# Performance work log

Measured on AMD Instinct MI355X. Metric: run time of the kernel, lower is better.

Reference implementation:

```python
import jax, jax.numpy as jnp
import numpy as np

D_EMB = 1024
N_HEAD = 16
D_K = D_EMB // N_HEAD


def setup_inputs() -> dict:
    key = jax.random.key(0)
    ks = jax.random.split(key, 11)
    B, S = 2, 2048
    s = 1.0 / np.sqrt(D_EMB)
    inp = {
        'Q': jax.random.normal(ks[0], (B, S, D_EMB), jnp.float32),
        'K': jax.random.normal(ks[1], (B, S, D_EMB), jnp.float32),
        'V': jax.random.normal(ks[2], (B, S, D_EMB), jnp.float32),
        'W_Q': jax.random.normal(ks[3], (D_EMB, D_EMB), jnp.float32) * s,
        'b_Q': jax.random.normal(ks[4], (D_EMB,), jnp.float32) * s,
        'W_K': jax.random.normal(ks[5], (D_EMB, D_EMB), jnp.float32) * s,
        'b_K': jax.random.normal(ks[6], (D_EMB,), jnp.float32) * s,
        'W_V': jax.random.normal(ks[7], (D_EMB, D_EMB), jnp.float32) * s,
        'b_V': jax.random.normal(ks[8], (D_EMB,), jnp.float32) * s,
        'W_O': jax.random.normal(ks[9], (D_EMB, D_EMB), jnp.float32) * s,
        'b_O': jax.random.normal(ks[10], (D_EMB,), jnp.float32) * s,
    }
    return inp


def _heads(x):
    # [B, S, D] -> [B, H, S, d_k]
    B, S, _ = x.shape
    return x.reshape(B, S, N_HEAD, D_K).transpose(0, 2, 1, 3)


def reference(Q, K, V, W_Q, b_Q, W_K, b_K, W_V, b_V, W_O, b_O):
    q = _heads(Q @ W_Q.T + b_Q)
    k = _heads(K @ W_K.T + b_K)
    v = _heads(V @ W_V.T + b_V)
    scale = 1.0 / jnp.sqrt(jnp.asarray(D_K, q.dtype))
    scores = jnp.einsum('bhqd,bhkd->bhqk', q, k) * scale  # [B,H,S,S]
    probs = jax.nn.softmax(scores, axis=-1)
    attn = jnp.einsum('bhqk,bhkd->bhqd', probs, v)
    B, H, S, d = attn.shape
    attn = attn.transpose(0, 2, 1, 3).reshape(B, S, H * d)
    return attn @ W_O.T + b_O
```

## Files before the change

kernel.cpp:

```cpp
#include <hip/hip_runtime.h>
#include <cstdint>
#include <cstddef>

#define S_LEN 2048
#define NH    16
#define DKH   64
#define DEMB  1024
#define MTOT  4096

typedef float f32x4 __attribute__((ext_vector_type(4)));
typedef __bf16 bf16x8 __attribute__((ext_vector_type(8)));
typedef _Float16 f16;
typedef f16 f16x2 __attribute__((ext_vector_type(2)));
typedef f16 f16x4 __attribute__((ext_vector_type(4)));
typedef unsigned short u16;
typedef unsigned int u32;
typedef u16 u16x8 __attribute__((ext_vector_type(8)));
typedef u16 u16x4 __attribute__((ext_vector_type(4)));

static __device__ __forceinline__ u16 f2bf(float f) {
  u32 u = __builtin_bit_cast(u32, f);
  u += 0x7fffu + ((u >> 16) & 1u);
  return (u16)(u >> 16);
}
static __device__ __forceinline__ float bf2f(u16 b) {
  return __builtin_bit_cast(float, ((u32)b) << 16);
}
static __device__ __forceinline__ bf16x8 ldfrag(const u16* p) {
  return __builtin_bit_cast(bf16x8, *(const u16x8*)p);
}
static __device__ __forceinline__ f16x4 ldfragh(const u16* p) {
  return __builtin_bit_cast(f16x4, *(const u16x4*)p);
}
static __device__ __forceinline__ f32x4 mfma16(bf16x8 a, bf16x8 b, f32x4 c) {
  return __builtin_amdgcn_mfma_f32_16x16x32_bf16(a, b, c, 0, 0, 0);
}
static __device__ __forceinline__ f32x4 mfmah(f16x4 a, f16x4 b, f32x4 c) {
  return __builtin_amdgcn_mfma_f32_16x16x16f16(a, b, c, 0, 0, 0);
}
static __device__ __forceinline__ void gl2lds16(const void* g, void* l) {
  __builtin_amdgcn_global_load_lds((__attribute__((address_space(1))) void*)g,
                                   (__attribute__((address_space(3))) void*)l,
                                   16, 0, 0);
}
static __device__ __forceinline__ f16x4 pkh4(float a, float b, float c, float d) {
  f16x2 lo = __builtin_bit_cast(f16x2, __builtin_amdgcn_cvt_pkrtz(a, b));
  f16x2 hi = __builtin_bit_cast(f16x2, __builtin_amdgcn_cvt_pkrtz(c, d));
  return __builtin_shufflevector(lo, hi, 0, 1, 2, 3);
}

#define SCL_Q (0.125f * 1.44269504088896340736f)

__global__ __launch_bounds__(256) void cvt_all(
    const float* __restrict__ wq, const float* __restrict__ wk,
    const float* __restrict__ wv, const float* __restrict__ wo,
    const float* __restrict__ q, const float* __restrict__ k,
    const float* __restrict__ v, u16* __restrict__ dW, u16* __restrict__ dA) {
  int b = blockIdx.x;
  const float* s; u16* d;
  if (b < 4096) {
    const int seg = b >> 10;
    s = (seg == 0) ? wq : (seg == 1) ? wk : (seg == 2) ? wv : wo;
    d = dW + (size_t)seg * (DEMB * DEMB);
    b &= 1023;
  } else {
    const int bb = b - 4096;
    const int seg = bb >> 12;
    s = (seg == 0) ? q : (seg == 1) ? k : v;
    d = dA + (size_t)seg * ((size_t)MTOT * DEMB);
    b = bb & 4095;
  }
  const int i = (b * 256 + threadIdx.x) * 4;
  f32x4 f = *(const f32x4*)(s + i);
  u16x4 o;
  o[0] = f2bf(f[0]); o[1] = f2bf(f[1]); o[2] = f2bf(f[2]); o[3] = f2bf(f[3]);
  *(u16x4*)(d + i) = o;
}

__global__ __launch_bounds__(256) void qkv_gemm(
    const u16* __restrict__ qin, const u16* __restrict__ kin,
    const u16* __restrict__ vin, const u16* __restrict__ W,
    const float* __restrict__ bq, const float* __restrict__ bk,
    const float* __restrict__ bv,
    u16* __restrict__ qh, u16* __restrict__ kh, u16* __restrict__ vt) {
  __shared__ __align__(16) u16 sA[128 * 32];
  __shared__ __align__(16) u16 sB[128 * 32];
  const int t = threadIdx.x;
  const int l = t & 63, w = t >> 6;
  const int ll = l & 15, lg = l >> 4;
  const int nb = blockIdx.x;
  const int mb = blockIdx.y;
  const int which = nb >> 3;
  const u16* A = (which == 0) ? qin : ((which == 1) ? kin : vin);
  const int wr = (w >> 1) * 64, wc = (w & 1) * 64;

  f32x4 acc[4][4] = {};

  for (int kt = 0; kt < 32; ++kt) {
    const int k0 = kt * 32;
    __syncthreads();
#pragma unroll
    for (int i = 0; i < 2; ++i) {
      const int c = i * 256 + t;
      const int row = c >> 2;
      const int gc = (c & 3) ^ ((row >> 1) & 3);
      gl2lds16(A + (size_t)(mb * 128 + row) * DEMB + k0 + gc * 8, &sA[c * 8]);
      gl2lds16(W + (size_t)(nb * 128 + row) * DEMB + k0 + gc * 8, &sB[c * 8]);
    }
    __syncthreads();

    bf16x8 af[4], bfr[4];
#pragma unroll
    for (int i2 = 0; i2 < 4; ++i2) {
      const int row = wr + i2 * 16 + ll;
      af[i2] = ldfrag(&sA[row * 32 + (lg ^ ((row >> 1) & 3)) * 8]);
    }
#pragma unroll
    for (int j2 = 0; j2 < 4; ++j2) {
      const int row = wc + j2 * 16 + ll;
      bfr[j2] = ldfrag(&sB[row * 32 + (lg ^ ((row >> 1) & 3)) * 8]);
    }
#pragma unroll
    for (int i2 = 0; i2 < 4; ++i2)
#pragma unroll
      for (int j2 = 0; j2 < 4; ++j2)
        acc[i2][j2] = mfma16(af[i2], bfr[j2], acc[i2][j2]);
  }

  const float* bias = (which == 0) ? bq : ((which == 1) ? bk : bv);
  const int b = (mb * 128) >> 11;

  if (which == 2) {
#pragma unroll
    for (int j2 = 0; j2 < 4; ++j2) {
      const int nl = (nb * 128 + wc + j2 * 16 + ll) & 1023;
      const int h = nl >> 6, dk = nl & 63;
      const float bb = bias[nl];
      u16* base = vt + ((size_t)((b * NH + h) * DKH + dk)) * S_LEN;
#pragma unroll
      for (int i2 = 0; i2 < 4; ++i2) {
        const int s = (mb * 128 + wr + i2 * 16 + lg * 4) & 2047;
        const f16x4 pk = pkh4(acc[i2][j2][0] + bb, acc[i2][j2][1] + bb,
                              acc[i2][j2][2] + bb, acc[i2][j2][3] + bb);
        *(u16x4*)&base[s] = __builtin_bit_cast(u16x4, pk);
      }
    }
  } else {
    u16* outp = (which == 0) ? qh : kh;
    const float scl = (which == 0) ? SCL_Q : 1.0f;
#pragma unroll
    for (int j2 = 0; j2 < 4; ++j2) {
      const int nl = (nb * 128 + wc + j2 * 16 + ll) & 1023;
      const int h = nl >> 6, dk = nl & 63;
      const float bb = bias[nl];
#pragma unroll
      for (int i2 = 0; i2 < 4; ++i2) {
#pragma unroll
        for (int r = 0; r < 4; ++r) {
          const int s = (mb * 128 + wr + i2 * 16 + lg * 4 + r) & 2047;
          const float val = (acc[i2][j2][r] + bb) * scl;
          outp[((size_t)((b * NH + h) * S_LEN + s)) * DKH + dk] = f2bf(val);
        }
      }
    }
  }
}

__global__ __launch_bounds__(256) void attn_kernel(
    const u16* __restrict__ qh, const u16* __restrict__ kh,
    const u16* __restrict__ vt, u16* __restrict__ opart,
    float* __restrict__ lpart) {
  __shared__ __align__(16) u16 sK[64 * 64];
  __shared__ __align__(16) u16 sV[64 * 64];
  const int t = threadIdx.x;
  const int l = t & 63, w = t >> 6;
  const int ll = l & 15, lg = l >> 4;
  const int qb = blockIdx.x >> 1;
  const int ks = blockIdx.x & 1;
  const int q_blk = qb * 128;
  const int bh = blockIdx.y;

  bf16x8 aq[2][2];
#pragma unroll
  for (int qt = 0; qt < 2; ++qt) {
    const u16* qbase = qh + ((size_t)bh * S_LEN + q_blk + w * 32 + qt * 16 + ll) * DKH;
    aq[qt][0] = ldfrag(qbase + lg * 8);
    aq[qt][1] = ldfrag(qbase + 32 + lg * 8);
  }

  f32x4 oT[2][4] = {};
  float l_part[2] = {0.f, 0.f};

  for (int kt = 0; kt < 16; ++kt) {
    const int kb0 = ks * 1024 + kt * 64;
    __syncthreads();
#pragma unroll
    for (int i = 0; i < 2; ++i) {
      const int c = i * 256 + t;
      const int row = c >> 3, gc = (c & 7) ^ (row & 7);
      gl2lds16(kh + ((size_t)bh * S_LEN + kb0 + row) * DKH + gc * 8,
               &sK[c * 8]);
      gl2lds16(vt + ((size_t)bh * DKH + row) * S_LEN + kb0 + gc * 8,
               &sV[c * 8]);
    }
    __syncthreads();

#pragma unroll
    for (int kbl = 0; kbl < 4; ++kbl) {
      const int krow = kbl * 16 + ll;
      const bf16x8 ak0 = ldfrag(&sK[krow * 64 + (lg ^ (ll & 7)) * 8]);
      const bf16x8 ak1 = ldfrag(&sK[krow * 64 + ((4 + lg) ^ (ll & 7)) * 8]);
      f32x4 s0 = {}, s1 = {};
      s0 = mfma16(ak0, aq[0][0], s0);
      s0 = mfma16(ak1, aq[0][1], s0);
      s1 = mfma16(ak0, aq[1][0], s1);
      s1 = mfma16(ak1, aq[1][1], s1);

      f16x4 bp0, bp1;
      {
        const float p0 = __builtin_amdgcn_exp2f(s0[0]);
        const float p1 = __builtin_amdgcn_exp2f(s0[1]);
        const float p2 = __builtin_amdgcn_exp2f(s0[2]);
        const float p3 = __builtin_amdgcn_exp2f(s0[3]);
        l_part[0] += (p0 + p1) + (p2 + p3);
        bp0 = pkh4(p0, p1, p2, p3);
      }
      {
        const float p0 = __builtin_amdgcn_exp2f(s1[0]);
        const float p1 = __builtin_amdgcn_exp2f(s1[1]);
        const float p2 = __builtin_amdgcn_exp2f(s1[2]);
        const float p3 = __builtin_amdgcn_exp2f(s1[3]);
        l_part[1] += (p0 + p1) + (p2 + p3);
        bp1 = pkh4(p0, p1, p2, p3);
      }

#pragma unroll
      for (int nt = 0; nt < 4; ++nt) {
        const int row = nt * 16 + ll;
        const int ch = (kbl * 2 + (lg >> 1)) ^ (ll & 7);
        const f16x4 av = ldfragh(&sV[row * 64 + ch * 8 + (lg & 1) * 4]);
        oT[0][nt] = mfmah(av, bp0, oT[0][nt]);
        oT[1][nt] = mfmah(av, bp1, oT[1][nt]);
      }
    }
  }

#pragma unroll
  for (int qt = 0; qt < 2; ++qt) {
    float lv = l_part[qt];
    lv += __shfl_xor(lv, 16, 64);
    lv += __shfl_xor(lv, 32, 64);
    const int srow = q_blk + w * 32 + qt * 16 + ll;
    u16* obase = opart + (((size_t)(ks * 32 + bh)) * S_LEN + srow) * DKH;
#pragma unroll
    for (int nt = 0; nt < 4; ++nt) {
      u16x4 o;
#pragma unroll
      for (int r = 0; r < 4; ++r) o[r] = f2bf(oT[qt][nt][r]);
      *(u16x4*)&obase[nt * 16 + lg * 4] = o;
    }
    if (lg == 0) lpart[(ks * 32 + bh) * S_LEN + srow] = lv;
  }
}

__global__ __launch_bounds__(256) void merge_ctx(
    const u16* __restrict__ op, const float* __restrict__ lp,
    u16* __restrict__ ctx) {
  const int idx = blockIdx.x * 256 + threadIdx.x;
  const int dk8 = idx & 7;
  const int q = (idx >> 3) & 2047;
  const int bh = idx >> 14;
  const float inv = 1.0f / (lp[bh * S_LEN + q] + lp[(32 + bh) * S_LEN + q]);
  const u16x8 a = *(const u16x8*)&op[((size_t)bh * S_LEN + q) * DKH + dk8 * 8];
  const u16x8 c = *(const u16x8*)&op[((size_t)(32 + bh) * S_LEN + q) * DKH + dk8 * 8];
  u16x8 o;
#pragma unroll
  for (int r = 0; r < 8; ++r) o[r] = f2bf((bf2f(a[r]) + bf2f(c[r])) * inv);
  const int b = bh >> 4, h = bh & 15;
  *(u16x8*)&ctx[((size_t)((b * S_LEN + q) * NH + h)) * DKH + dk8 * 8] = o;
}

__global__ __launch_bounds__(256) void out_gemm(
    const u16* __restrict__ Am, const u16* __restrict__ W,
    const float* __restrict__ bo, float* __restrict__ out) {
  __shared__ __align__(16) u16 sA[64 * 64];
  __shared__ __align__(16) u16 sB[64 * 64];
  const int t = threadIdx.x;
  const int l = t & 63, w = t >> 6;
  const int ll = l & 15, lg = l >> 4;
  const int nb = blockIdx.x;
  const int mb = blockIdx.y;
  const int wr = (w >> 1) * 32, wc = (w & 1) * 32;

  f32x4 acc[2][2] = {};
  for (int kt = 0; kt < 16; ++kt) {
    const int k0 = kt * 64;
    __syncthreads();
#pragma unroll
    for (int i = 0; i < 2; ++i) {
      const int c = i * 256 + t;
      const int row = c >> 3;
      const int gc = (c & 7) ^ (row & 7);
      gl2lds16(Am + (size_t)(mb * 64 + row) * DEMB + k0 + gc * 8, &sA[c * 8]);
      gl2lds16(W + (size_t)(nb * 64 + row) * DEMB + k0 + gc * 8, &sB[c * 8]);
    }
    __syncthreads();
#pragma unroll
    for (int sub = 0; sub < 2; ++sub) {
      bf16x8 af[2], bfr[2];
#pragma unroll
      for (int i2 = 0; i2 < 2; ++i2) {
        const int row = wr + i2 * 16 + ll;
        af[i2] = ldfrag(&sA[row * 64 + ((sub * 4 + lg) ^ (row & 7)) * 8]);
      }
#pragma unroll
      for (int j2 = 0; j2 < 2; ++j2) {
        const int row = wc + j2 * 16 + ll;
        bfr[j2] = ldfrag(&sB[row * 64 + ((sub * 4 + lg) ^ (row & 7)) * 8]);
      }
#pragma unroll
      for (int i2 = 0; i2 < 2; ++i2)
#pragma unroll
        for (int j2 = 0; j2 < 2; ++j2)
          acc[i2][j2] = mfma16(af[i2], bfr[j2], acc[i2][j2]);
    }
  }

#pragma unroll
  for (int j2 = 0; j2 < 2; ++j2) {
    const int ncol = nb * 64 + wc + j2 * 16 + ll;
    const float bb = bo[ncol];
#pragma unroll
    for (int i2 = 0; i2 < 2; ++i2) {
#pragma unroll
      for (int r = 0; r < 4; ++r) {
        const int mrow = mb * 64 + wr + i2 * 16 + lg * 4 + r;
        out[(size_t)mrow * DEMB + ncol] = acc[i2][j2][r] + bb;
      }
    }
  }
}

extern "C" void kernel_launch(void* const* d_in, const int* in_sizes, int n_in,
                              void* d_out, int out_size, void* d_ws,
                              size_t ws_size, hipStream_t stream) {
  (void)in_sizes; (void)n_in; (void)out_size; (void)ws_size;
  const float* Q  = (const float*)d_in[0];
  const float* K  = (const float*)d_in[1];
  const float* V  = (const float*)d_in[2];
  const float* WQ = (const float*)d_in[3];
  const float* bQ = (const float*)d_in[4];
  const float* WK = (const float*)d_in[5];
  const float* bK = (const float*)d_in[6];
  const float* WV = (const float*)d_in[7];
  const float* bV = (const float*)d_in[8];
  const float* WO = (const float*)d_in[9];
  const float* bO = (const float*)d_in[10];
  float* out = (float*)d_out;

  u16* ws   = (u16*)d_ws;
  u16* Wqkv = ws;
  u16* Wo   = Wqkv + 3072 * 1024;
  u16* qin  = Wo + 1024 * 1024;
  u16* kin  = qin + (size_t)MTOT * DEMB;
  u16* vin  = kin + (size_t)MTOT * DEMB;
  u16* qh   = vin + (size_t)MTOT * DEMB;
  u16* kh   = qh + 32 * 2048 * 64;
  u16* vt   = kh + 32 * 2048 * 64;
  u16* ctx  = vt + 32 * 2048 * 64;
  u16* opart   = qin;
  float* lpart = (float*)Wqkv;

  cvt_all<<<16384, 256, 0, stream>>>(WQ, WK, WV, WO, Q, K, V, Wqkv, qin);

  qkv_gemm<<<dim3(24, 32), 256, 0, stream>>>(qin, kin, vin, Wqkv, bQ, bK, bV,
                                             qh, kh, vt);
  attn_kernel<<<dim3(32, 32), 256, 0, stream>>>(qh, kh, vt, opart, lpart);
  merge_ctx<<<2048, 256, 0, stream>>>(opart, lpart, ctx);
  out_gemm<<<dim3(16, 64), 256, 0, stream>>>(ctx, Wo, bO, out);
}
```

Baseline: 235.3 us.

## Double-buffer attention and output GEMM, enlarge K tiles and block sizes

The QKV GEMM moves from a 32-wide to a 64-wide K tile, halving the number of barrier-separated load/compute rounds. The attention kernel now uses 512-thread blocks covering 256 queries with double-buffered K/V tiles, so loads overlap MFMA work. The output GEMM grows to 128x64 tiles with double-buffered LDS. Together these aim to hide global-to-LDS latency and reduce synchronisation, at the cost of more LDS per block and possibly lower occupancy.

After: 233.4 us. No clear change (-0.8%).

```diff
diff --git a/kernel.cpp b/kernel.cpp
--- a/kernel.cpp
+++ b/kernel.cpp
@@ -83,8 +83,8 @@
     const float* __restrict__ bq, const float* __restrict__ bk,
     const float* __restrict__ bv,
     u16* __restrict__ qh, u16* __restrict__ kh, u16* __restrict__ vt) {
-  __shared__ __align__(16) u16 sA[128 * 32];
-  __shared__ __align__(16) u16 sB[128 * 32];
+  __shared__ __align__(16) u16 sA[128 * 64];
+  __shared__ __align__(16) u16 sB[128 * 64];
   const int t = threadIdx.x;
   const int l = t & 63, w = t >> 6;
   const int ll = l & 15, lg = l >> 4;
@@ -96,35 +96,38 @@
 
   f32x4 acc[4][4] = {};
 
-  for (int kt = 0; kt < 32; ++kt) {
-    const int k0 = kt * 32;
-    __syncthreads();
-#pragma unroll
-    for (int i = 0; i < 2; ++i) {
+  for (int kt = 0; kt < 16; ++kt) {
+    const int k0 = kt * 64;
+    __syncthreads();
+#pragma unroll
+    for (int i = 0; i < 4; ++i) {
       const int c = i * 256 + t;
-      const int row = c >> 2;
-      const int gc = (c & 3) ^ ((row >> 1) & 3);
+      const int row = c >> 3;
+      const int gc = (c & 7) ^ (row & 7);
       gl2lds16(A + (size_t)(mb * 128 + row) * DEMB + k0 + gc * 8, &sA[c * 8]);
       gl2lds16(W + (size_t)(nb * 128 + row) * DEMB + k0 + gc * 8, &sB[c * 8]);
     }
     __syncthreads();
 
-    bf16x8 af[4], bfr[4];
-#pragma unroll
-    for (int i2 = 0; i2 < 4; ++i2) {
-      const int row = wr + i2 * 16 + ll;
-      af[i2] = ldfrag(&sA[row * 32 + (lg ^ ((row >> 1) & 3)) * 8]);
-    }
-#pragma unroll
-    for (int j2 = 0; j2 < 4; ++j2) {
-      const int row = wc + j2 * 16 + ll;
-      bfr[j2] = ldfrag(&sB[row * 32 + (lg ^ ((row >> 1) & 3)) * 8]);
-    }
-#pragma unroll
-    for (int i2 = 0; i2 < 4; ++i2)
-#pragma unroll
-      for (int j2 = 0; j2 < 4; ++j2)
-        acc[i2][j2] = mfma16(af[i2], bfr[j2], acc[i2][j2]);
+#pragma unroll
+    for (int kk = 0; kk < 2; ++kk) {
+      bf16x8 af[4], bfr[4];
+#pragma unroll
+      for (int i2 = 0; i2 < 4; ++i2) {
+        const int row = wr + i2 * 16 + ll;
+        af[i2] = ldfrag(&sA[row * 64 + ((kk * 4 + lg) ^ (row & 7)) * 8]);
+      }
+#pragma unroll
+      for (int j2 = 0; j2 < 4; ++j2) {
+        const int row = wc + j2 * 16 + ll;
+        bfr[j2] = ldfrag(&sB[row * 64 + ((kk * 4 + lg) ^ (row & 7)) * 8]);
+      }
+#pragma unroll
+      for (int i2 = 0; i2 < 4; ++i2)
+#pragma unroll
+        for (int j2 = 0; j2 < 4; ++j2)
+          acc[i2][j2] = mfma16(af[i2], bfr[j2], acc[i2][j2]);
+    }
   }
 
   const float* bias = (which == 0) ? bq : ((which == 1) ? bk : bv);
@@ -166,24 +169,25 @@
   }
 }
 
-__global__ __launch_bounds__(256) void attn_kernel(
+__global__ __launch_bounds__(512, 4) void attn_kernel(
     const u16* __restrict__ qh, const u16* __restrict__ kh,
     const u16* __restrict__ vt, u16* __restrict__ opart,
     float* __restrict__ lpart) {
-  __shared__ __align__(16) u16 sK[64 * 64];
-  __shared__ __align__(16) u16 sV[64 * 64];
+  __shared__ __align__(16) u16 sK0[64 * 64], sK1[64 * 64];
+  __shared__ __align__(16) u16 sV0[64 * 64], sV1[64 * 64];
   const int t = threadIdx.x;
   const int l = t & 63, w = t >> 6;
   const int ll = l & 15, lg = l >> 4;
   const int qb = blockIdx.x >> 1;
   const int ks = blockIdx.x & 1;
-  const int q_blk = qb * 128;
+  const int q_blk = qb * 256;
   const int bh = blockIdx.y;
 
   bf16x8 aq[2][2];
 #pragma unroll
   for (int qt = 0; qt < 2; ++qt) {
-    const u16* qbase = qh + ((size_t)bh * S_LEN + q_blk + w * 32 + qt * 16 + ll) * DKH;
+    const u16* qbase =
+        qh + ((size_t)bh * S_LEN + q_blk + w * 32 + qt * 16 + ll) * DKH;
     aq[qt][0] = ldfrag(qbase + lg * 8);
     aq[qt][1] = ldfrag(qbase + 32 + lg * 8);
   }
@@ -191,25 +195,22 @@
   f32x4 oT[2][4] = {};
   float l_part[2] = {0.f, 0.f};
 
-  for (int kt = 0; kt < 16; ++kt) {
-    const int kb0 = ks * 1024 + kt * 64;
-    __syncthreads();
-#pragma unroll
-    for (int i = 0; i < 2; ++i) {
-      const int c = i * 256 + t;
-      const int row = c >> 3, gc = (c & 7) ^ (row & 7);
-      gl2lds16(kh + ((size_t)bh * S_LEN + kb0 + row) * DKH + gc * 8,
-               &sK[c * 8]);
-      gl2lds16(vt + ((size_t)bh * DKH + row) * S_LEN + kb0 + gc * 8,
-               &sV[c * 8]);
-    }
-    __syncthreads();
-
+  const int strow = t >> 3;
+  const int sgc = (t & 7) ^ (strow & 7);
+  const u16* kstg = kh + ((size_t)bh * S_LEN + ks * 1024 + strow) * DKH + sgc * 8;
+  const u16* vstg = vt + ((size_t)bh * DKH + strow) * S_LEN + ks * 1024 + sgc * 8;
+
+  auto stg = [&](int kt, u16* dK, u16* dV) {
+    gl2lds16(kstg + (size_t)kt * 64 * DKH, dK + t * 8);
+    gl2lds16(vstg + kt * 64, dV + t * 8);
+  };
+
+  auto compute = [&](const u16* cK, const u16* cV) {
 #pragma unroll
     for (int kbl = 0; kbl < 4; ++kbl) {
       const int krow = kbl * 16 + ll;
-      const bf16x8 ak0 = ldfrag(&sK[krow * 64 + (lg ^ (ll & 7)) * 8]);
-      const bf16x8 ak1 = ldfrag(&sK[krow * 64 + ((4 + lg) ^ (ll & 7)) * 8]);
+      const bf16x8 ak0 = ldfrag(&cK[krow * 64 + (lg ^ (ll & 7)) * 8]);
+      const bf16x8 ak1 = ldfrag(&cK[krow * 64 + ((4 + lg) ^ (ll & 7)) * 8]);
       f32x4 s0 = {}, s1 = {};
       s0 = mfma16(ak0, aq[0][0], s0);
       s0 = mfma16(ak1, aq[0][1], s0);
@@ -238,11 +239,22 @@
       for (int nt = 0; nt < 4; ++nt) {
         const int row = nt * 16 + ll;
         const int ch = (kbl * 2 + (lg >> 1)) ^ (ll & 7);
-        const f16x4 av = ldfragh(&sV[row * 64 + ch * 8 + (lg & 1) * 4]);
+        const f16x4 av = ldfragh(&cV[row * 64 + ch * 8 + (lg & 1) * 4]);
         oT[0][nt] = mfmah(av, bp0, oT[0][nt]);
         oT[1][nt] = mfmah(av, bp1, oT[1][nt]);
       }
     }
+  };
+
+  stg(0, sK0, sV0);
+  __syncthreads();
+  for (int kt2 = 0; kt2 < 8; ++kt2) {
+    stg(2 * kt2 + 1, sK1, sV1);
+    compute(sK0, sV0);
+    __syncthreads();
+    if (kt2 < 7) stg(2 * kt2 + 2, sK0, sV0);
+    compute(sK1, sV1);
+    __syncthreads();
   }
 
 #pragma unroll
@@ -250,8 +262,8 @@
     float lv = l_part[qt];
     lv += __shfl_xor(lv, 16, 64);
     lv += __shfl_xor(lv, 32, 64);
-    const int srow = q_blk + w * 32 + qt * 16 + ll;
-    u16* obase = opart + (((size_t)(ks * 32 + bh)) * S_LEN + srow) * DKH;
+    const int orow = q_blk + w * 32 + qt * 16 + ll;
+    u16* obase = opart + (((size_t)(ks * 32 + bh)) * S_LEN + orow) * DKH;
 #pragma unroll
     for (int nt = 0; nt < 4; ++nt) {
       u16x4 o;
@@ -259,7 +271,7 @@
       for (int r = 0; r < 4; ++r) o[r] = f2bf(oT[qt][nt][r]);
       *(u16x4*)&obase[nt * 16 + lg * 4] = o;
     }
-    if (lg == 0) lpart[(ks * 32 + bh) * S_LEN + srow] = lv;
+    if (lg == 0) lpart[(ks * 32 + bh) * S_LEN + orow] = lv;
   }
 }
 
@@ -283,47 +295,61 @@
 __global__ __launch_bounds__(256) void out_gemm(
     const u16* __restrict__ Am, const u16* __restrict__ W,
     const float* __restrict__ bo, float* __restrict__ out) {
-  __shared__ __align__(16) u16 sA[64 * 64];
-  __shared__ __align__(16) u16 sB[64 * 64];
+  __shared__ __align__(16) u16 sA0[128 * 64], sA1[128 * 64];
+  __shared__ __align__(16) u16 sB0[64 * 64], sB1[64 * 64];
   const int t = threadIdx.x;
   const int l = t & 63, w = t >> 6;
   const int ll = l & 15, lg = l >> 4;
   const int nb = blockIdx.x;
   const int mb = blockIdx.y;
-  const int wr = (w >> 1) * 32, wc = (w & 1) * 32;
-
-  f32x4 acc[2][2] = {};
-  for (int kt = 0; kt < 16; ++kt) {
+  const int wr = (w >> 1) * 64, wc = (w & 1) * 32;
+
+  f32x4 acc[4][2] = {};
+
+  auto stg = [&](int kt, u16* dA, u16* dB) {
     const int k0 = kt * 64;
-    __syncthreads();
-#pragma unroll
-    for (int i = 0; i < 2; ++i) {
+#pragma unroll
+    for (int i = 0; i < 4; ++i) {
       const int c = i * 256 + t;
       const int row = c >> 3;
       const int gc = (c & 7) ^ (row & 7);
-      gl2lds16(Am + (size_t)(mb * 64 + row) * DEMB + k0 + gc * 8, &sA[c * 8]);
-      gl2lds16(W + (size_t)(nb * 64 + row) * DEMB + k0 + gc * 8, &sB[c * 8]);
-    }
-    __syncthreads();
-#pragma unroll
-    for (int sub = 0; sub < 2; ++sub) {
-      bf16x8 af[2], bfr[2];
-#pragma unroll
-      for (int i2 = 0; i2 < 2; ++i2) {
+      gl2lds16(Am + (size_t)(mb * 128 + row) * DEMB + k0 + gc * 8, dA + c * 8);
+      if (i < 2)
+        gl2lds16(W + (size_t)(nb * 64 + row) * DEMB + k0 + gc * 8, dB + c * 8);
+    }
+  };
+
+  auto comp = [&](const u16* cA, const u16* cB) {
+#pragma unroll
+    for (int kk = 0; kk < 2; ++kk) {
+      bf16x8 af[4], bfr[2];
+#pragma unroll
+      for (int i2 = 0; i2 < 4; ++i2) {
         const int row = wr + i2 * 16 + ll;
-        af[i2] = ldfrag(&sA[row * 64 + ((sub * 4 + lg) ^ (row & 7)) * 8]);
+        af[i2] = ldfrag(&cA[row * 64 + ((kk * 4 + lg) ^ (row & 7)) * 8]);
       }
 #pragma unroll
       for (int j2 = 0; j2 < 2; ++j2) {
         const int row = wc + j2 * 16 + ll;
-        bfr[j2] = ldfrag(&sB[row * 64 + ((sub * 4 + lg) ^ (row & 7)) * 8]);
-      }
-#pragma unroll
-      for (int i2 = 0; i2 < 2; ++i2)
+        bfr[j2] = ldfrag(&cB[row * 64 + ((kk * 4 + lg) ^ (row & 7)) * 8]);
+      }
+#pragma unroll
+      for (int i2 = 0; i2 < 4; ++i2)
 #pragma unroll
         for (int j2 = 0; j2 < 2; ++j2)
           acc[i2][j2] = mfma16(af[i2], bfr[j2], acc[i2][j2]);
     }
+  };
+
+  stg(0, sA0, sB0);
+  __syncthreads();
+  for (int kt2 = 0; kt2 < 8; ++kt2) {
+    stg(2 * kt2 + 1, sA1, sB1);
+    comp(sA0, sB0);
+    __syncthreads();
+    if (kt2 < 7) stg(2 * kt2 + 2, sA0, sB0);
+    comp(sA1, sB1);
+    __syncthreads();
   }
 
 #pragma unroll
@@ -331,10 +357,10 @@
     const int ncol = nb * 64 + wc + j2 * 16 + ll;
     const float bb = bo[ncol];
 #pragma unroll
-    for (int i2 = 0; i2 < 2; ++i2) {
+    for (int i2 = 0; i2 < 4; ++i2) {
 #pragma unroll
       for (int r = 0; r < 4; ++r) {
-        const int mrow = mb * 64 + wr + i2 * 16 + lg * 4 + r;
+        const int mrow = mb * 128 + wr + i2 * 16 + lg * 4 + r;
         out[(size_t)mrow * DEMB + ncol] = acc[i2][j2][r] + bb;
       }
     }
@@ -375,7 +401,7 @@
 
   qkv_gemm<<<dim3(24, 32), 256, 0, stream>>>(qin, kin, vin, Wqkv, bQ, bK, bV,
                                              qh, kh, vt);
-  attn_kernel<<<dim3(32, 32), 256, 0, stream>>>(qh, kh, vt, opart, lpart);
+  attn_kernel<<<dim3(16, 32), 512, 0, stream>>>(qh, kh, vt, opart, lpart);
   merge_ctx<<<2048, 256, 0, stream>>>(opart, lpart, ctx);
-  out_gemm<<<dim3(16, 64), 256, 0, stream>>>(ctx, Wo, bO, out);
-}
+  out_gemm<<<dim3(16, 32), 256, 0, stream>>>(ctx, Wo, bO, out);
+}
```
